# Performance work log

Measured on AMD Instinct MI355X. Metric: run time of the kernel, lower is better.

Reference implementation:

```python
import jax, jax.numpy as jnp
import numpy as np

B, IN, H = 16384, 1024, 1024


def setup_inputs() -> dict:
    key = jax.random.key(0)
    ks = jax.random.split(key, 16)
    stdv = 1.0 / np.sqrt(H)
    u = lambda k, shape: jax.random.uniform(k, shape, jnp.float32, -stdv, stdv)
    return {
        "input": jax.random.normal(ks[0], (B, IN), jnp.float32),
        "prev_h": jax.random.normal(ks[1], (B, H), jnp.float32),
        "prev_c": jax.random.normal(ks[2], (B, H), jnp.float32),
        "weight_xi": u(ks[3], (IN, H)), "weight_hi": u(ks[4], (H, H)),
        "weight_xf": u(ks[5], (IN, H)), "weight_hf": u(ks[6], (H, H)),
        "weight_xu": u(ks[7], (IN, H)), "weight_hu": u(ks[8], (H, H)),
        "weight_xo": u(ks[9], (IN, H)), "weight_ho": u(ks[10], (H, H)),
        "bias_i": u(ks[11], (H,)), "bias_f": u(ks[12], (H,)),
        "bias_o": u(ks[13], (H,)), "bias_u": u(ks[14], (H,)),
    }


def reference(input, prev_h, prev_c,
              weight_xi, weight_hi, weight_xf, weight_hf,
              weight_xu, weight_hu, weight_xo, weight_ho,
              bias_i, bias_f, bias_o, bias_u):
    i = jax.nn.sigmoid(input @ weight_xi + prev_h @ weight_hi + bias_i)
    f = jax.nn.sigmoid(input @ weight_xf + prev_h @ weight_hf + bias_f)
    o = jax.nn.sigmoid(input @ weight_xo + prev_h @ weight_ho + bias_o)
    u = jnp.tanh(input @ weight_xu + prev_h @ weight_hu + bias_u)
    c = f * prev_c + i * u
    h = o * jnp.tanh(c)
    return (h, c)
```

## Files before the change

### kernel.cpp

```cpp
#include <hip/hip_runtime.h>
#include <hip/hip_bf16.h>
#include <stdint.h>
#include <type_traits>


typedef short bf16x8 __attribute__((ext_vector_type(8)));
typedef unsigned short u16x8 __attribute__((ext_vector_type(8)));
typedef float f32x4 __attribute__((ext_vector_type(4)));

__device__ __forceinline__ unsigned short f2bf(float f) {
    union { float f; uint32_t u; } v; v.f = f;
    uint32_t r = v.u + 0x7FFFu + ((v.u >> 16) & 1u);
    return (unsigned short)(r >> 16);
}

__device__ __forceinline__ float fsig(float x) { return 1.0f / (1.0f + __expf(-x)); }
__device__ __forceinline__ float ftanh(float x) { return 2.0f * fsig(2.0f * x) - 1.0f; }

__global__ __launch_bounds__(256) void pack_a_kernel(const float* __restrict__ input,
                                                     const float* __restrict__ prev_h,
                                                     unsigned short* __restrict__ Apk) {
    long idx = (long)blockIdx.x * 256 + threadIdx.x;
    long e0 = idx * 8;
    int b = (int)(e0 >> 11);
    int k = (int)(e0 & 2047);
    const float* src = (k < 1024) ? (input + (size_t)b * 1024 + k)
                                  : (prev_h + (size_t)b * 1024 + (k - 1024));
    float4 lo = *(const float4*)src;
    float4 hi = *(const float4*)(src + 4);
    u16x8 o;
    o[0] = f2bf(lo.x); o[1] = f2bf(lo.y); o[2] = f2bf(lo.z); o[3] = f2bf(lo.w);
    o[4] = f2bf(hi.x); o[5] = f2bf(hi.y); o[6] = f2bf(hi.z); o[7] = f2bf(hi.w);
    *(u16x8*)(Apk + e0) = o;
}

__global__ __launch_bounds__(256) void pack_b_kernel(
        const float* __restrict__ wxi, const float* __restrict__ wxf,
        const float* __restrict__ wxo, const float* __restrict__ wxu,
        const float* __restrict__ whi, const float* __restrict__ whf,
        const float* __restrict__ who, const float* __restrict__ whu,
        unsigned short* __restrict__ Bpk) {
    int idx = blockIdx.x * 256 + threadIdx.x;
    int g  = idx >> 18;
    int r  = idx & 262143;
    int kc = r >> 10;
    int j  = r & 1023;
    const float* wx = (g == 0) ? wxi : (g == 1) ? wxf : (g == 2) ? wxo : wxu;
    const float* wh = (g == 0) ? whi : (g == 1) ? whf : (g == 2) ? who : whu;
    int k0 = kc * 8;
    const float* src = (k0 < 1024) ? (wx + (size_t)k0 * 1024 + j)
                                   : (wh + (size_t)(k0 - 1024) * 1024 + j);
    u16x8 o;
#pragma unroll
    for (int t = 0; t < 8; ++t) o[t] = f2bf(src[(size_t)t * 1024]);
    *(u16x8*)(Bpk + (((size_t)(g * 1024 + j)) << 11) + k0) = o;
}


#define GLL(gp, lp) __builtin_amdgcn_global_load_lds( \
        (__attribute__((address_space(1))) void*)(gp), \
        (__attribute__((address_space(3))) void*)(lp), 16, 0, 0)

__global__ __launch_bounds__(512, 2) void lstm_gemm_kernel(
        const unsigned short* __restrict__ Apk,
        const unsigned short* __restrict__ Bpk,
        const float* __restrict__ prev_c,
        const float* __restrict__ bi, const float* __restrict__ bf_,
        const float* __restrict__ bo, const float* __restrict__ bu,
        float* __restrict__ out_h, float* __restrict__ out_c) {
    __shared__ __align__(16) unsigned char smem[131072];
    const int tid = threadIdx.x;
    const int w = tid >> 6, l = tid & 63;
    const int lr = l & 15, s4 = l >> 4;
    const int wm = w >> 2, wq = w & 3;

    const int bid = blockIdx.x;
    const int sw = ((bid & 7) << 7) + (bid >> 3);
    const int tileRow = sw & 63, tileCol = sw >> 6;
    const int rowBase = tileRow * 256;
    const int jBase = tileCol * 64;

    const int swr = ((s4 ^ ((lr >> 1) & 3)) << 4);

    int aoff[8], boff[4];
#pragma unroll
    for (int m = 0; m < 8; ++m) aoff[m] = (wm * 128 + m * 16 + lr) * 64 + swr;
#pragma unroll
    for (int g = 0; g < 4; ++g) boff[g] = 16384 + (g * 64 + wq * 16 + lr) * 64 + swr;

    const int slot = (l & 3) ^ ((l >> 3) & 3);
    const int rloc = w * 16 + (l >> 2);
    const unsigned short* aSrc0 = Apk + (size_t)(rowBase + rloc) * 2048 + slot * 8;
    const unsigned short* aSrc1 = Apk + (size_t)(rowBase + 128 + rloc) * 2048 + slot * 8;
    const int br0 = rloc, br1 = 128 + rloc;
    const unsigned short* bSrc0 = Bpk + (((size_t)((br0 >> 6) * 1024 + jBase + (br0 & 63))) << 11) + slot * 8;
    const unsigned short* bSrc1 = Bpk + (((size_t)((br1 >> 6) * 1024 + jBase + (br1 & 63))) << 11) + slot * 8;
    const int aDst0 = w * 1024;
    const int aDst1 = 8192 + w * 1024;
    const int bDst0 = 16384 + w * 1024;
    const int bDst1 = 24576 + w * 1024;

#define STAGE(T) do { const int _bb = ((T) & 3) * 32768; \
        GLL(aSrc0 + (size_t)(T) * 32, smem + _bb + aDst0); \
        GLL(aSrc1 + (size_t)(T) * 32, smem + _bb + aDst1); \
        GLL(bSrc0 + (size_t)(T) * 32, smem + _bb + bDst0); \
        GLL(bSrc1 + (size_t)(T) * 32, smem + _bb + bDst1); } while (0)

    f32x4 acc[8][4];
    const f32x4 vzero = {0.f, 0.f, 0.f, 0.f};
#pragma unroll
    for (int m = 0; m < 8; ++m)
#pragma unroll
        for (int g = 0; g < 4; ++g) acc[m][g] = vzero;

    bf16x8 fra[12], frb[12];

    auto ldfr = [&](int t, bf16x8 (&dst)[12]) {
        const int bn = (t & 3) * 32768;
#pragma unroll
        for (int m = 0; m < 8; ++m) dst[m] = *(const bf16x8*)(smem + bn + aoff[m]);
#pragma unroll
        for (int g = 0; g < 4; ++g) dst[8 + g] = *(const bf16x8*)(smem + bn + boff[g]);
    };

    STAGE(0); STAGE(1); STAGE(2);
    asm volatile("s_waitcnt vmcnt(8)" ::: "memory");
    __builtin_amdgcn_s_barrier();
    asm volatile("" ::: "memory");
    ldfr(0, fra);

    auto body = [&](int t, auto vnc, auto stgc, bf16x8 (&cur)[12], bf16x8 (&nxt)[12]) {
        constexpr int VN = decltype(vnc)::value;
        constexpr bool STG = decltype(stgc)::value;
        if constexpr (STG) STAGE(t + 3);
        if constexpr (VN >= 0) {
            if constexpr (VN == 8)      asm volatile("s_waitcnt vmcnt(8)" ::: "memory");
            else if constexpr (VN == 4) asm volatile("s_waitcnt vmcnt(4)" ::: "memory");
            else                        asm volatile("s_waitcnt vmcnt(0)" ::: "memory");
            asm volatile("s_waitcnt lgkmcnt(0)" ::: "memory");
            __builtin_amdgcn_s_barrier();
            asm volatile("" ::: "memory");
            ldfr(t + 1, nxt);
        }
        __builtin_amdgcn_s_setprio(1);
#pragma unroll
        for (int m = 0; m < 8; ++m)
#pragma unroll
            for (int g = 0; g < 4; ++g)
                acc[m][g] = __builtin_amdgcn_mfma_f32_16x16x32_bf16(cur[m], cur[8 + g], acc[m][g], 0, 0, 0);
        __builtin_amdgcn_s_setprio(0);
        if constexpr (VN >= 0) {
            __builtin_amdgcn_sched_group_barrier(0x100, 12, 0);
            __builtin_amdgcn_sched_group_barrier(0x8,   32, 0);
        }
    };

    using ci8 = std::integral_constant<int, 8>;
    using ci4 = std::integral_constant<int, 4>;
    using ci0 = std::integral_constant<int, 0>;
    using cim = std::integral_constant<int, -1>;
    using bt_ = std::integral_constant<bool, true>;
    using bf_c = std::integral_constant<bool, false>;

#pragma unroll 1
    for (int t = 0; t < 60; t += 2) {
        body(t,     ci8{}, bt_{}, fra, frb);
        body(t + 1, ci8{}, bt_{}, frb, fra);
    }
    body(60, ci8{}, bt_{},  fra, frb);
    body(61, ci4{}, bf_c{}, frb, fra);
    body(62, ci0{}, bf_c{}, fra, frb);
    body(63, cim{}, bf_c{}, frb, fra);

    const int colIdx = jBase + wq * 16 + lr;
    const float vbi = bi[colIdx], vbf = bf_[colIdx], vbo = bo[colIdx], vbu = bu[colIdx];
    const int rowB = rowBase + wm * 128 + s4 * 4;
#pragma unroll
    for (int m = 0; m < 8; ++m) {
#pragma unroll
        for (int tt = 0; tt < 4; ++tt) {
            const size_t idx = (size_t)(rowB + m * 16 + tt) * 1024 + colIdx;
            float zi = acc[m][0][tt] + vbi;
            float zf = acc[m][1][tt] + vbf;
            float zo = acc[m][2][tt] + vbo;
            float zu = acc[m][3][tt] + vbu;
            float iv = fsig(zi), fv = fsig(zf), ov = fsig(zo), uv = ftanh(zu);
            float cv = fv * prev_c[idx] + iv * uv;
            out_c[idx] = cv;
            out_h[idx] = ov * ftanh(cv);
        }
    }
#undef STAGE
}

extern "C" void kernel_launch(void* const* d_in, const int* in_sizes, int n_in,
                              void* d_out, int out_size, void* d_ws, size_t ws_size,
                              hipStream_t stream) {
    const float* input  = (const float*)d_in[0];
    const float* prev_h = (const float*)d_in[1];
    const float* prev_c = (const float*)d_in[2];
    const float* wxi = (const float*)d_in[3];
    const float* whi = (const float*)d_in[4];
    const float* wxf = (const float*)d_in[5];
    const float* whf = (const float*)d_in[6];
    const float* wxu = (const float*)d_in[7];
    const float* whu = (const float*)d_in[8];
    const float* wxo = (const float*)d_in[9];
    const float* who = (const float*)d_in[10];
    const float* bi  = (const float*)d_in[11];
    const float* bf_ = (const float*)d_in[12];
    const float* bo  = (const float*)d_in[13];
    const float* bu  = (const float*)d_in[14];

    unsigned short* Apk = (unsigned short*)d_ws;
    unsigned short* Bpk = (unsigned short*)((char*)d_ws + (size_t)67108864);

    float* out_h = (float*)d_out;
    float* out_c = out_h + (size_t)16384 * 1024;

    pack_a_kernel<<<dim3(16384), dim3(256), 0, stream>>>(input, prev_h, Apk);
    pack_b_kernel<<<dim3(4096), dim3(256), 0, stream>>>(wxi, wxf, wxo, wxu,
                                                        whi, whf, who, whu, Bpk);
    lstm_gemm_kernel<<<dim3(1024), dim3(512), 0, stream>>>(Apk, Bpk, prev_c,
                                                           bi, bf_, bo, bu, out_h, out_c);
}
```

Measured before the change: 351.3 us.

## Load B fragments directly from global into registers, stage only A in LDS

Stops staging the B (weight) tile through shared memory: each wave now loads its B fragments straight from global memory into registers one step ahead, and only the A tile goes through LDS via global_load_lds. LDS drops from 128KB to 64KB and the prefetch depth changes from three stages ahead to two. This removes LDS traffic and LDS reads for B, but B is now duplicated across the two wm waves that share columns. It also puts global-load latency directly on the register path, which relies on the one-step prefetch and L2 hits to hide it.

```diff
diff --git a/kernel.cpp b/kernel.cpp
--- a/kernel.cpp
+++ b/kernel.cpp
@@ -61,6 +61,9 @@
         (__attribute__((address_space(1))) void*)(gp), \
         (__attribute__((address_space(3))) void*)(lp), 16, 0, 0)
 
+#define BAR() do { asm volatile("" ::: "memory"); __builtin_amdgcn_s_barrier(); \
+                   asm volatile("" ::: "memory"); } while (0)
+
 __global__ __launch_bounds__(512, 2) void lstm_gemm_kernel(
         const unsigned short* __restrict__ Apk,
         const unsigned short* __restrict__ Bpk,
@@ -68,7 +71,7 @@
         const float* __restrict__ bi, const float* __restrict__ bf_,
         const float* __restrict__ bo, const float* __restrict__ bu,
         float* __restrict__ out_h, float* __restrict__ out_c) {
-    __shared__ __align__(16) unsigned char smem[131072];
+    __shared__ __align__(16) unsigned char smem[65536];
     const int tid = threadIdx.x;
     const int w = tid >> 6, l = tid & 63;
     const int lr = l & 15, s4 = l >> 4;
@@ -81,30 +84,24 @@
     const int jBase = tileCol * 64;
 
     const int swr = ((s4 ^ ((lr >> 1) & 3)) << 4);
-
-    int aoff[8], boff[4];
-#pragma unroll
-    for (int m = 0; m < 8; ++m) aoff[m] = (wm * 128 + m * 16 + lr) * 64 + swr;
-#pragma unroll
-    for (int g = 0; g < 4; ++g) boff[g] = 16384 + (g * 64 + wq * 16 + lr) * 64 + swr;
+    const int aofBase = (wm * 128 + lr) * 64 + swr;
+
+    const int colIdx = jBase + wq * 16 + lr;
+    const unsigned short* bPtr0 = Bpk + (((size_t)(0 * 1024 + colIdx)) << 11) + s4 * 8;
+    const unsigned short* bPtr1 = Bpk + (((size_t)(1 * 1024 + colIdx)) << 11) + s4 * 8;
+    const unsigned short* bPtr2 = Bpk + (((size_t)(2 * 1024 + colIdx)) << 11) + s4 * 8;
+    const unsigned short* bPtr3 = Bpk + (((size_t)(3 * 1024 + colIdx)) << 11) + s4 * 8;
 
     const int slot = (l & 3) ^ ((l >> 3) & 3);
     const int rloc = w * 16 + (l >> 2);
     const unsigned short* aSrc0 = Apk + (size_t)(rowBase + rloc) * 2048 + slot * 8;
     const unsigned short* aSrc1 = Apk + (size_t)(rowBase + 128 + rloc) * 2048 + slot * 8;
-    const int br0 = rloc, br1 = 128 + rloc;
-    const unsigned short* bSrc0 = Bpk + (((size_t)((br0 >> 6) * 1024 + jBase + (br0 & 63))) << 11) + slot * 8;
-    const unsigned short* bSrc1 = Bpk + (((size_t)((br1 >> 6) * 1024 + jBase + (br1 & 63))) << 11) + slot * 8;
     const int aDst0 = w * 1024;
     const int aDst1 = 8192 + w * 1024;
-    const int bDst0 = 16384 + w * 1024;
-    const int bDst1 = 24576 + w * 1024;
-
-#define STAGE(T) do { const int _bb = ((T) & 3) * 32768; \
+
+#define STAGE_A(T) do { const int _bb = ((T) & 3) * 16384; \
         GLL(aSrc0 + (size_t)(T) * 32, smem + _bb + aDst0); \
-        GLL(aSrc1 + (size_t)(T) * 32, smem + _bb + aDst1); \
-        GLL(bSrc0 + (size_t)(T) * 32, smem + _bb + bDst0); \
-        GLL(bSrc1 + (size_t)(T) * 32, smem + _bb + bDst1); } while (0)
+        GLL(aSrc1 + (size_t)(T) * 32, smem + _bb + aDst1); } while (0)
 
     f32x4 acc[8][4];
     const f32x4 vzero = {0.f, 0.f, 0.f, 0.f};
@@ -113,66 +110,69 @@
 #pragma unroll
         for (int g = 0; g < 4; ++g) acc[m][g] = vzero;
 
-    bf16x8 fra[12], frb[12];
-
-    auto ldfr = [&](int t, bf16x8 (&dst)[12]) {
-        const int bn = (t & 3) * 32768;
-#pragma unroll
-        for (int m = 0; m < 8; ++m) dst[m] = *(const bf16x8*)(smem + bn + aoff[m]);
-#pragma unroll
-        for (int g = 0; g < 4; ++g) dst[8 + g] = *(const bf16x8*)(smem + bn + boff[g]);
+    bf16x8 aE[8], aO[8], bE[4], bO[4];
+
+    auto ldA = [&](int t, bf16x8 (&dst)[8]) {
+        const unsigned char* p = smem + (t & 3) * 16384 + aofBase;
+#pragma unroll
+        for (int m = 0; m < 8; ++m) dst[m] = *(const bf16x8*)(p + m * 1024);
     };
-
-    STAGE(0); STAGE(1); STAGE(2);
-    asm volatile("s_waitcnt vmcnt(8)" ::: "memory");
-    __builtin_amdgcn_s_barrier();
-    asm volatile("" ::: "memory");
-    ldfr(0, fra);
-
-    auto body = [&](int t, auto vnc, auto stgc, bf16x8 (&cur)[12], bf16x8 (&nxt)[12]) {
+    auto ldB = [&](int t, bf16x8 (&dst)[4]) {
+        const size_t o = (size_t)t * 32;
+        dst[0] = *(const bf16x8*)(bPtr0 + o);
+        dst[1] = *(const bf16x8*)(bPtr1 + o);
+        dst[2] = *(const bf16x8*)(bPtr2 + o);
+        dst[3] = *(const bf16x8*)(bPtr3 + o);
+    };
+
+    STAGE_A(0); STAGE_A(1);
+    ldB(0, bE);
+    asm volatile("s_waitcnt vmcnt(0)" ::: "memory");
+    BAR();
+    ldA(0, aE);
+
+    auto slice = [&](int t, auto vnc, auto stgc, auto nxtc,
+                     bf16x8 (&ac)[8], bf16x8 (&an)[8],
+                     bf16x8 (&bc)[4], bf16x8 (&bn)[4]) {
         constexpr int VN = decltype(vnc)::value;
         constexpr bool STG = decltype(stgc)::value;
-        if constexpr (STG) STAGE(t + 3);
-        if constexpr (VN >= 0) {
-            if constexpr (VN == 8)      asm volatile("s_waitcnt vmcnt(8)" ::: "memory");
-            else if constexpr (VN == 4) asm volatile("s_waitcnt vmcnt(4)" ::: "memory");
-            else                        asm volatile("s_waitcnt vmcnt(0)" ::: "memory");
-            asm volatile("s_waitcnt lgkmcnt(0)" ::: "memory");
-            __builtin_amdgcn_s_barrier();
-            asm volatile("" ::: "memory");
-            ldfr(t + 1, nxt);
-        }
+        constexpr bool NXT = decltype(nxtc)::value;
+        if constexpr (NXT) ldB(t + 1, bn);
+        if constexpr (STG) STAGE_A(t + 2);
+        if constexpr (VN == 6)      asm volatile("s_waitcnt vmcnt(6)" ::: "memory");
+        else if constexpr (VN == 4) asm volatile("s_waitcnt vmcnt(4)" ::: "memory");
+        else                        asm volatile("s_waitcnt vmcnt(0)" ::: "memory");
+        BAR();
+        asm volatile("s_waitcnt lgkmcnt(0)" ::: "memory");
+        __builtin_amdgcn_sched_barrier(0);
+        if constexpr (NXT) ldA(t + 1, an);
         __builtin_amdgcn_s_setprio(1);
 #pragma unroll
         for (int m = 0; m < 8; ++m)
 #pragma unroll
             for (int g = 0; g < 4; ++g)
-                acc[m][g] = __builtin_amdgcn_mfma_f32_16x16x32_bf16(cur[m], cur[8 + g], acc[m][g], 0, 0, 0);
+                acc[m][g] = __builtin_amdgcn_mfma_f32_16x16x32_bf16(ac[m], bc[g], acc[m][g], 0, 0, 0);
         __builtin_amdgcn_s_setprio(0);
-        if constexpr (VN >= 0) {
-            __builtin_amdgcn_sched_group_barrier(0x100, 12, 0);
-            __builtin_amdgcn_sched_group_barrier(0x8,   32, 0);
+        if constexpr (NXT) {
+            __builtin_amdgcn_sched_group_barrier(0x100, 8, 0);
+            __builtin_amdgcn_sched_group_barrier(0x8,  32, 0);
         }
     };
 
-    using ci8 = std::integral_constant<int, 8>;
-    using ci4 = std::integral_constant<int, 4>;
-    using ci0 = std::integral_constant<int, 0>;
-    using cim = std::integral_constant<int, -1>;
-    using bt_ = std::integral_constant<bool, true>;
-    using bf_c = std::integral_constant<bool, false>;
+    using c6 = std::integral_constant<int, 6>;
+    using c4 = std::integral_constant<int, 4>;
+    using c0 = std::integral_constant<int, 0>;
+    using bT = std::integral_constant<bool, true>;
+    using bF = std::integral_constant<bool, false>;
 
 #pragma unroll 1
-    for (int t = 0; t < 60; t += 2) {
-        body(t,     ci8{}, bt_{}, fra, frb);
-        body(t + 1, ci8{}, bt_{}, frb, fra);
+    for (int t = 0; t < 62; t += 2) {
+        slice(t,     c6{}, bT{}, bT{}, aE, aO, bE, bO);
+        slice(t + 1, c6{}, bT{}, bT{}, aO, aE, bO, bE);
     }
-    body(60, ci8{}, bt_{},  fra, frb);
-    body(61, ci4{}, bf_c{}, frb, fra);
-    body(62, ci0{}, bf_c{}, fra, frb);
-    body(63, cim{}, bf_c{}, frb, fra);
-
-    const int colIdx = jBase + wq * 16 + lr;
+    slice(62, c4{}, bF{}, bT{}, aE, aO, bE, bO);
+    slice(63, c0{}, bF{}, bF{}, aO, aE, bO, bE);
+
     const float vbi = bi[colIdx], vbf = bf_[colIdx], vbo = bo[colIdx], vbu = bu[colIdx];
     const int rowB = rowBase + wm * 128 + s4 * 4;
 #pragma unroll
@@ -190,7 +190,7 @@
             out_h[idx] = ov * ftanh(cv);
         }
     }
-#undef STAGE
+#undef STAGE_A
 }
 
 extern "C" void kernel_launch(void* const* d_in, const int* in_sizes, int n_in,
```

New measurement: 414.3 us. 1.18x slower.
